# Kernel optimization log

Hardware: AMD Instinct MI355X
Metric: run time of the kernel (lower is better)

The kernel has to match this reference:

```python
import jax, jax.numpy as jnp
import numpy as np

B, H, W, C = 16, 64, 64, 256
NH = 8          # num_heads
WS = 8          # window size (8,8) from shift=2
HID = 1024      # mlp hidden = 4*C
EPS = 1e-5


def _rel_index():
    # relative_position_index exactly as in the torch module (meshgrid 'ij')
    ch = np.arange(WS)
    coords = np.stack(np.meshgrid(ch, ch, indexing='ij'))          # (2, WS, WS)
    flat = coords.reshape(2, -1)                                    # (2, N)
    rel = flat[:, :, None] - flat[:, None, :]                       # (2, N, N)
    rel = rel.transpose(1, 2, 0).astype(np.int64)                   # (N, N, 2)
    rel[..., 0] += WS - 1
    rel[..., 1] += WS - 1
    rel[..., 0] *= 2 * WS - 1
    return jnp.asarray(rel.sum(-1))                                 # (N, N)


def _ln(x, w, b):
    m = x.mean(-1, keepdims=True)
    v = jnp.mean((x - m) ** 2, axis=-1, keepdims=True)
    return (x - m) / jnp.sqrt(v + EPS) * w + b


def setup_inputs() -> dict:
    key = jax.random.key(0)
    ks = jax.random.split(key, 16)
    std = 0.02
    n_bias = (2 * WS - 1) * (2 * WS - 1)  # 225
    return {
        'x': jax.random.normal(ks[0], (B, H * W, C), jnp.float32),
        'norm1_w': jnp.ones((C,), jnp.float32),
        'norm1_b': jnp.zeros((C,), jnp.float32),
        'qkv_w': jax.random.normal(ks[1], (3 * C, C), jnp.float32) * std,
        'qkv_b': jnp.zeros((3 * C,), jnp.float32),
        'rel_bias': jax.random.normal(ks[2], (n_bias, NH), jnp.float32) * std,
        'proj_w': jax.random.normal(ks[3], (C, C), jnp.float32) * std,
        'proj_b': jnp.zeros((C,), jnp.float32),
        'norm2_w': jnp.ones((C,), jnp.float32),
        'norm2_b': jnp.zeros((C,), jnp.float32),
        'fc1_w': jax.random.normal(ks[4], (HID, C), jnp.float32) * std,
        'fc1_b': jnp.zeros((HID,), jnp.float32),
        'dw_w': jax.random.normal(ks[5], (3, 3, 1, HID), jnp.float32) * std,  # HWIO depthwise
        'dw_b': jnp.zeros((HID,), jnp.float32),
        'fc2_w': jax.random.normal(ks[6], (C, HID), jnp.float32) * std,
        'fc2_b': jnp.zeros((C,), jnp.float32),
    }


def reference(x, norm1_w, norm1_b, qkv_w, qkv_b, rel_bias, proj_w, proj_b,
              norm2_w, norm2_b, fc1_w, fc1_b, dw_w, dw_b, fc2_w, fc2_b):
    S = (H // WS) * (W // WS)   # num windows = 64
    N = WS * WS                 # tokens per window = 64
    shortcut = x
    h = _ln(x, norm1_w, norm1_b).reshape(B, H, W, C)
    # window partition -> (B, S, N, C), then permute to (B, N, S, C)
    hw = (h.reshape(B, H // WS, WS, W // WS, WS, C)
            .transpose(0, 1, 3, 2, 4, 5)
            .reshape(B, S, N, C))
    xw = hw.transpose(0, 2, 1, 3)            # (B, N, S, C)
    # qkv over flattened (N*S) tokens; heads split the S*C feature dim
    xf = xw.reshape(B, N * S, C)
    qkv = xf @ qkv_w.T + qkv_b               # (B, N*S, 3C)
    qkv = qkv.reshape(B, N, 3, NH, S * C // NH).transpose(2, 0, 3, 1, 4)
    q, k, v = qkv[0], qkv[1], qkv[2]         # (B, NH, N, S*C/NH)
    scale = (C // NH) ** -0.5
    attn = jnp.einsum('bhnd,bhmd->bhnm', q, k) * scale   # (B, NH, N, N)
    idx = _rel_index()
    bias = rel_bias[idx.reshape(-1)].reshape(N, N, NH).transpose(2, 0, 1)
    attn = jax.nn.softmax(attn + bias[None], axis=-1)
    out = jnp.einsum('bhnm,bhmd->bhnd', attn, v)         # (B, NH, N, S*C/NH)
    out = out.transpose(0, 2, 1, 3).reshape(B, N * S, C)
    out = (out @ proj_w.T + proj_b).reshape(B, N, S, C).transpose(0, 2, 1, 3)  # (B,S,N,C)
    # window reverse -> (B, H*W, C)
    xr = (out.reshape(B, H // WS, W // WS, WS, WS, C)
             .transpose(0, 1, 3, 2, 4, 5)
             .reshape(B, H * W, C))
    x = shortcut + xr
    # conv-based MLP (eval mode, dropout = identity)
    y = _ln(x, norm2_w, norm2_b).reshape(B, H, H, C)      # NHWC
    y = jnp.einsum('bhwc,oc->bhwo', y, fc1_w) + fc1_b     # 1x1 conv
    y = jax.lax.conv_general_dilated(
        y, dw_w, (1, 1), 'SAME',
        dimension_numbers=('NHWC', 'HWIO', 'NHWC'),
        feature_group_count=HID) + dw_b
    y = jax.nn.gelu(y, approximate=False)
    y = jnp.einsum('bhwo,co->bhwc', y, fc2_w) + fc2_b     # 1x1 conv
    return x + y.reshape(B, H * W, C)
```

## Files before the change

### kernel.cpp

```cpp
#include <hip/hip_runtime.h>
#include <hip/hip_bf16.h>
#include <cstdint>
#include <cstddef>

#define B_     16
#define HW_    4096
#define C_     256
#define NH_    8
#define S_     64
#define N_     64
#define C3_    768
#define HID_   1024
#define DHEAD_ 2048
#define EPS_   1e-5f

using u16 = unsigned short;
using u32 = unsigned int;

typedef __attribute__((ext_vector_type(8))) short bf16x8;
typedef __attribute__((ext_vector_type(4))) float f32x4;

__device__ __forceinline__ float bf2f(u16 u) {
  union { float f; u32 i; } x; x.i = ((u32)u) << 16; return x.f;
}
__device__ __forceinline__ u16 f2bf(float f) {
  union { float f; u32 i; } x; x.f = f;
  u32 r = (x.i + 0x7FFFu + ((x.i >> 16) & 1u)) >> 16;
  return (u16)r;
}

__device__ __forceinline__ void gload_lds16(const u16* g, u16* l) {
  __builtin_amdgcn_global_load_lds(
      (const __attribute__((address_space(1))) unsigned int*)g,
      (__attribute__((address_space(3))) unsigned int*)l, 16, 0, 0);
}

__launch_bounds__(256)
__global__ void f2bf_kernel(const float* __restrict__ in, u16* __restrict__ out) {
  int i = blockIdx.x * 256 + threadIdx.x;
  float4 v = ((const float4*)in)[i];
  ushort4 o = {f2bf(v.x), f2bf(v.y), f2bf(v.z), f2bf(v.w)};
  ((ushort4*)out)[i] = o;
}

__launch_bounds__(256)
__global__ void ln_kernel(const float* __restrict__ in, const float* __restrict__ w,
                          const float* __restrict__ bias, u16* __restrict__ out,
                          int b_base) {
  int wave = threadIdx.x >> 6;
  int lane = threadIdx.x & 63;
  int t = blockIdx.x * 4 + wave;
  int b = b_base + (t >> 12);
  int r = t & 4095;
  int n = r >> 6, s = r & 63;
  int hw = (((s >> 3) << 3) + (n >> 3)) * 64 + ((s & 7) << 3) + (n & 7);
  size_t src_row = ((size_t)b << 12) + hw;
  float4 v = ((const float4*)(in + src_row * C_))[lane];
  float sum = v.x + v.y + v.z + v.w;
#pragma unroll
  for (int off = 32; off; off >>= 1) sum += __shfl_xor(sum, off);
  float mean = sum * (1.0f / C_);
  float4 d = {v.x - mean, v.y - mean, v.z - mean, v.w - mean};
  float ss = d.x * d.x + d.y * d.y + d.z * d.z + d.w * d.w;
#pragma unroll
  for (int off = 32; off; off >>= 1) ss += __shfl_xor(ss, off);
  float rstd = rsqrtf(ss * (1.0f / C_) + EPS_);
  float4 w4 = ((const float4*)w)[lane];
  float4 b4 = ((const float4*)bias)[lane];
  ushort4 o;
  o.x = f2bf(d.x * rstd * w4.x + b4.x);
  o.y = f2bf(d.y * rstd * w4.y + b4.y);
  o.z = f2bf(d.z * rstd * w4.z + b4.z);
  o.w = f2bf(d.w * rstd * w4.w + b4.w);
  ((ushort4*)(out + (size_t)t * C_))[lane] = o;
}

template<int K_, int J_, int EPI>
__launch_bounds__(256, 2)
__global__ void gemm_mfma(const u16* __restrict__ A, const u16* __restrict__ Wb,
                          const float* __restrict__ bias, u16* __restrict__ outB,
                          float* __restrict__ outF, const float* __restrict__ res,
                          int m_base, u16* __restrict__ qb, u16* __restrict__ kb,
                          u16* __restrict__ vt) {
  constexpr int NT = K_ / 64;
  __shared__ u16 As[2][128 * 64];
  __shared__ u16 Bs[2][128 * 64];
  int tid = threadIdx.x;
  int wid = tid >> 6, lane = tid & 63;
  int n0 = blockIdx.x * 128;
  int m0 = blockIdx.y * 128;
  int wr = wid >> 1, wc = wid & 1;
  f32x4 acc[4][4] = {};

  int srow8 = lane >> 3;
  int sslot = lane & 7;

#define GSTAGE(buf, t)                                                         \
  {                                                                            \
    int k0g = (t) * 64;                                                        \
    _Pragma("unroll")                                                          \
    for (int r = 0; r < 4; ++r) {                                              \
      int row = wid * 32 + r * 8 + srow8;                                      \
      int cb = ((sslot ^ srow8) << 4);                                         \
      gload_lds16(A + (size_t)(m0 + row) * K_ + k0g + (cb >> 1),               \
                  &As[buf][(wid * 32 + r * 8) * 64]);                          \
      gload_lds16(Wb + (size_t)(n0 + row) * K_ + k0g + (cb >> 1),              \
                  &Bs[buf][(wid * 32 + r * 8) * 64]);                          \
    }                                                                          \
  }

  GSTAGE(0, 0);
  asm volatile("s_waitcnt vmcnt(0)" ::: "memory");
  __builtin_amdgcn_sched_barrier(0);
  __builtin_amdgcn_s_barrier();
  __builtin_amdgcn_sched_barrier(0);

#pragma unroll
  for (int t = 0; t < NT; ++t) {
    if (t + 1 < NT) GSTAGE((t + 1) & 1, t + 1);
    const u16* as = As[t & 1];
    const u16* bs = Bs[t & 1];
#pragma unroll
    for (int kk = 0; kk < 2; ++kk) {
      bf16x8 afr[4], bfr[4];
#pragma unroll
      for (int mf = 0; mf < 4; ++mf) {
        int ra = wr * 64 + mf * 16 + (lane & 15);
        int cb = (((kk * 4 + (lane >> 4)) ^ (ra & 7)) << 4);
        afr[mf] = *(const bf16x8*)&as[ra * 64 + (cb >> 1)];
      }
#pragma unroll
      for (int nf = 0; nf < 4; ++nf) {
        int rb = wc * 64 + nf * 16 + (lane & 15);
        int cb = (((kk * 4 + (lane >> 4)) ^ (rb & 7)) << 4);
        bfr[nf] = *(const bf16x8*)&bs[rb * 64 + (cb >> 1)];
      }
#pragma unroll
      for (int mf = 0; mf < 4; ++mf)
#pragma unroll
        for (int nf = 0; nf < 4; ++nf)
          acc[mf][nf] = __builtin_amdgcn_mfma_f32_16x16x32_bf16(afr[mf], bfr[nf], acc[mf][nf], 0, 0, 0);
    }
    asm volatile("s_waitcnt vmcnt(0)" ::: "memory");
    __builtin_amdgcn_sched_barrier(0);
    __builtin_amdgcn_s_barrier();
    __builtin_amdgcn_sched_barrier(0);
  }
#undef GSTAGE

#pragma unroll
  for (int nf = 0; nf < 4; ++nf) {
    int col = n0 + wc * 64 + nf * 16 + (lane & 15);
    float bv = bias[col];
#pragma unroll
    for (int mf = 0; mf < 4; ++mf) {
#pragma unroll
      for (int j = 0; j < 4; ++j) {
        int m = m0 + wr * 64 + mf * 16 + (lane >> 4) * 4 + j;
        float v = acc[mf][nf][j] + bv;
        if (EPI == 0) {
          outB[(size_t)m * J_ + col] = f2bf(v);
        } else if (EPI == 2) {
          size_t o = (size_t)(m_base + m) * C_ + col;
          outF[o] += v;
        } else {
          int b_rel = m >> 12, nn = (m >> 6) & 63, s = m & 63;
          int f = s * 768 + col;
          int part = f >> 14, hh = (f >> 11) & 7, d = f & 2047;
          u16 val = f2bf(v);
          size_t bh = (size_t)b_rel * 8 + hh;
          if (part == 0)      qb[(bh * 64 + nn) * 2048 + d] = val;
          else if (part == 1) kb[(bh * 64 + nn) * 2048 + d] = val;
          else                vt[(bh * 2048 + d) * 64 + nn] = val;
        }
      }
    }
  }
}

__launch_bounds__(256, 2)
__global__ void proj_ln_fused(const u16* __restrict__ A, const u16* __restrict__ Wb,
                              const float* __restrict__ bias, const float* __restrict__ res,
                              float* __restrict__ outF, const float* __restrict__ ln_w,
                              const float* __restrict__ ln_b, u16* __restrict__ h2,
                              int m_base) {
  __shared__ u16 As[2][64 * 64];
  __shared__ u16 Bs[2][256 * 64];
  int tid = threadIdx.x;
  int wid = tid >> 6, lane = tid & 63;
  int m0 = blockIdx.x * 64;
  f32x4 acc[4][4] = {};
  int srow8 = lane >> 3, sslot = lane & 7;

#define PSTAGE(buf, t)                                                         \
  {                                                                            \
    int k0g = (t) * 64;                                                        \
    int cb = ((sslot ^ srow8) << 4);                                           \
    _Pragma("unroll")                                                          \
    for (int r = 0; r < 2; ++r) {                                              \
      int row = wid * 16 + r * 8 + srow8;                                      \
      gload_lds16(A + (size_t)(m0 + row) * 256 + k0g + (cb >> 1),              \
                  &As[buf][(wid * 16 + r * 8) * 64]);                          \
    }                                                                          \
    _Pragma("unroll")                                                          \
    for (int r = 0; r < 8; ++r) {                                              \
      int row = wid * 64 + r * 8 + srow8;                                      \
      gload_lds16(Wb + (size_t)row * 256 + k0g + (cb >> 1),                    \
                  &Bs[buf][(wid * 64 + r * 8) * 64]);                          \
    }                                                                          \
  }

  PSTAGE(0, 0);
  asm volatile("s_waitcnt vmcnt(0)" ::: "memory");
  __builtin_amdgcn_sched_barrier(0);
  __builtin_amdgcn_s_barrier();
  __builtin_amdgcn_sched_barrier(0);

#pragma unroll
  for (int t = 0; t < 4; ++t) {
    if (t + 1 < 4) PSTAGE((t + 1) & 1, t + 1);
    const u16* as = As[t & 1];
    const u16* bs = Bs[t & 1];
#pragma unroll
    for (int kk = 0; kk < 2; ++kk) {
      bf16x8 afr[4], bfr[4];
#pragma unroll
      for (int mf = 0; mf < 4; ++mf) {
        int ra = mf * 16 + (lane & 15);
        int cb = (((kk * 4 + (lane >> 4)) ^ (ra & 7)) << 4);
        afr[mf] = *(const bf16x8*)&as[ra * 64 + (cb >> 1)];
      }
#pragma unroll
      for (int nf = 0; nf < 4; ++nf) {
        int rb = wid * 64 + nf * 16 + (lane & 15);
        int cb = (((kk * 4 + (lane >> 4)) ^ (rb & 7)) << 4);
        bfr[nf] = *(const bf16x8*)&bs[rb * 64 + (cb >> 1)];
      }
#pragma unroll
      for (int mf = 0; mf < 4; ++mf)
#pragma unroll
        for (int nf = 0; nf < 4; ++nf)
          acc[mf][nf] = __builtin_amdgcn_mfma_f32_16x16x32_bf16(afr[mf], bfr[nf], acc[mf][nf], 0, 0, 0);
    }
    asm volatile("s_waitcnt vmcnt(0)" ::: "memory");
    __builtin_amdgcn_sched_barrier(0);
    __builtin_amdgcn_s_barrier();
    __builtin_amdgcn_sched_barrier(0);
  }
#undef PSTAGE

  float (*red)[8] = (float (*)[8])As;

#pragma unroll
  for (int mf = 0; mf < 4; ++mf) {
#pragma unroll
    for (int j = 0; j < 4; ++j) {
      int m = m0 + mf * 16 + (lane >> 4) * 4 + j;
      int gm = m_base + m;
      int b = gm >> 12, nn = (gm >> 6) & 63, s = gm & 63;
      int hw = (((s >> 3) << 3) + (nn >> 3)) * 64 + ((s & 7) << 3) + (nn & 7);
      size_t rowo = (((size_t)b << 12) + hw) * C_;
      float s1 = 0.f, s2 = 0.f;
#pragma unroll
      for (int nf = 0; nf < 4; ++nf) {
        int col = wid * 64 + nf * 16 + (lane & 15);
        float v = acc[mf][nf][j] + bias[col] + res[rowo + col];
        acc[mf][nf][j] = v;
        outF[rowo + col] = v;
        s1 += v; s2 += v * v;
      }
#pragma unroll
      for (int off = 1; off < 16; off <<= 1) {
        s1 += __shfl_xor(s1, off);
        s2 += __shfl_xor(s2, off);
      }
      if ((lane & 15) == 0) {
        int rr = mf * 16 + (lane >> 4) * 4 + j;
        red[rr][wid * 2] = s1;
        red[rr][wid * 2 + 1] = s2;
      }
    }
  }
  __syncthreads();

#pragma unroll
  for (int mf = 0; mf < 4; ++mf) {
#pragma unroll
    for (int j = 0; j < 4; ++j) {
      int rr = mf * 16 + (lane >> 4) * 4 + j;
      float sum = red[rr][0] + red[rr][2] + red[rr][4] + red[rr][6];
      float ssq = red[rr][1] + red[rr][3] + red[rr][5] + red[rr][7];
      float mean = sum * (1.0f / C_);
      float var = ssq * (1.0f / C_) - mean * mean;
      float rstd = rsqrtf(var + EPS_);
      int m = m0 + rr;
      int b_rel = m >> 12, nn = (m >> 6) & 63, s = m & 63;
      int hw = (((s >> 3) << 3) + (nn >> 3)) * 64 + ((s & 7) << 3) + (nn & 7);
      size_t ho = (((size_t)b_rel << 12) + hw) * C_;
#pragma unroll
      for (int nf = 0; nf < 4; ++nf) {
        int col = wid * 64 + nf * 16 + (lane & 15);
        float nv = (acc[mf][nf][j] - mean) * rstd * ln_w[col] + ln_b[col];
        h2[ho + col] = f2bf(nv);
      }
    }
  }
}

__launch_bounds__(256)
__global__ void attn_mfma(const u16* __restrict__ qb, const u16* __restrict__ kb,
                          const u16* __restrict__ vt, const float* __restrict__ rel_bias,
                          u16* __restrict__ outp) {
  __shared__ u16 bufA[4096];
  __shared__ u16 bufB[4096];
  int bh = blockIdx.x;
  int h = bh & 7;
  int b_rel = bh >> 3;
  int tid = threadIdx.x;
  int w = tid >> 6, lane = tid & 63;
  int l3 = lane >> 3, l7 = lane & 7;
  const u16* qg = qb + (size_t)bh * 64 * 2048;
  const u16* kg = kb + (size_t)bh * 64 * 2048;
  const u16* vg = vt + (size_t)bh * 2048 * 64;

  f32x4 acc[4] = {};
  for (int k0 = 0; k0 < 2048; k0 += 64) {
#pragma unroll
    for (int r = 0; r < 2; ++r) {
      int row = w * 16 + r * 8 + l3;
      int sc = (l7 ^ (row & 7)) * 8;
      gload_lds16(qg + (size_t)row * 2048 + k0 + sc, &bufA[(w * 16 + r * 8) * 64]);
      gload_lds16(kg + (size_t)row * 2048 + k0 + sc, &bufB[(w * 16 + r * 8) * 64]);
    }
    __syncthreads();
    int rowq = w * 16 + (lane & 15);
#pragma unroll
    for (int ks = 0; ks < 2; ++ks) {
      bf16x8 aq = *(const bf16x8*)&bufA[rowq * 64 + (((ks * 4 + (lane >> 4)) ^ (rowq & 7)) << 3)];
#pragma unroll
      for (int cf = 0; cf < 4; ++cf) {
        int m = cf * 16 + (lane & 15);
        bf16x8 bk = *(const bf16x8*)&bufB[m * 64 + (((ks * 4 + (lane >> 4)) ^ (m & 7)) << 3)];
        acc[cf] = __builtin_amdgcn_mfma_f32_16x16x32_bf16(aq, bk, acc[cf], 0, 0, 0);
      }
    }
    __syncthreads();
  }

  const float scale = 0.17677669529663688f;
#pragma unroll
  for (int j = 0; j < 4; ++j) {
    int r = w * 16 + (lane >> 4) * 4 + j;
    int i1 = r >> 3, j1 = r & 7;
    float v[4];
#pragma unroll
    for (int cf = 0; cf < 4; ++cf) {
      int c = cf * 16 + (lane & 15);
      int idx = (i1 - (c >> 3) + 7) * 15 + (j1 - (c & 7) + 7);
      v[cf] = acc[cf][j] * scale + rel_bias[idx * NH_ + h];
    }
    float mx = fmaxf(fmaxf(v[0], v[1]), fmaxf(v[2], v[3]));
#pragma unroll
    for (int off = 8; off; off >>= 1) mx = fmaxf(mx, __shfl_xor(mx, off));
    float sm = 0.f;
#pragma unroll
    for (int cf = 0; cf < 4; ++cf) { v[cf] = __expf(v[cf] - mx); sm += v[cf]; }
#pragma unroll
    for (int off = 8; off; off >>= 1) sm += __shfl_xor(sm, off);
    float inv = 1.0f / sm;
#pragma unroll
    for (int cf = 0; cf < 4; ++cf) {
      int c = cf * 16 + (lane & 15);
      bufA[r * 64 + (c ^ ((r & 7) << 3))] = f2bf(v[cf] * inv);
    }
  }
  __syncthreads();

  bf16x8 pa[2];
  {
    int n = w * 16 + (lane & 15);
#pragma unroll
    for (int ks = 0; ks < 2; ++ks)
      pa[ks] = *(const bf16x8*)&bufA[n * 64 + ((ks * 32 + (lane >> 4) * 8) ^ ((n & 7) << 3))];
  }

  for (int d0 = 0; d0 < 2048; d0 += 64) {
#pragma unroll
    for (int r = 0; r < 2; ++r) {
      int drow = w * 16 + r * 8 + l3;
      int sc = (l7 ^ (drow & 7)) * 8;
      gload_lds16(vg + (size_t)(d0 + drow) * 64 + sc, &bufB[(w * 16 + r * 8) * 64]);
    }
    __syncthreads();
    f32x4 o[4] = {};
#pragma unroll
    for (int ks = 0; ks < 2; ++ks)
#pragma unroll
      for (int cf = 0; cf < 4; ++cf) {
        int d = cf * 16 + (lane & 15);
        bf16x8 bv = *(const bf16x8*)&bufB[d * 64 + (((ks * 4 + (lane >> 4)) ^ (d & 7)) << 3)];
        o[cf] = __builtin_amdgcn_mfma_f32_16x16x32_bf16(pa[ks], bv, o[cf], 0, 0, 0);
      }
#pragma unroll
    for (int cf = 0; cf < 4; ++cf) {
      int f = h * 2048 + d0 + cf * 16 + (lane & 15);
      int s = f >> 8, c = f & 255;
#pragma unroll
      for (int j = 0; j < 4; ++j) {
        int n = w * 16 + (lane >> 4) * 4 + j;
        outp[(((size_t)b_rel * 64 + n) * 64 + s) * 256 + c] = f2bf(o[cf][j]);
      }
    }
    __syncthreads();
  }
}

__launch_bounds__(256)
__global__ void dwconv_gelu(const u16* __restrict__ y1, const float* __restrict__ dw_w,
                            const float* __restrict__ dw_b, u16* __restrict__ y2) {
  int bid = blockIdx.x;
  int wt = bid & 31, ht = (bid >> 5) & 15, b = bid >> 9;
  int h0 = ht * 4, w0 = wt * 2;
  int c0 = threadIdx.x * 4;

  float4 wv[9];
#pragma unroll
  for (int i = 0; i < 9; ++i) wv[i] = *(const float4*)&dw_w[i * HID_ + c0];

  ushort4 in[6][4];
#pragma unroll
  for (int ii = 0; ii < 6; ++ii) {
    int hh = h0 + ii - 1;
#pragma unroll
    for (int jj = 0; jj < 4; ++jj) {
      int ww = w0 + jj - 1;
      if ((unsigned)hh < 64u && (unsigned)ww < 64u)
        in[ii][jj] = *(const ushort4*)(y1 + ((size_t)((b << 12) + hh * 64 + ww)) * HID_ + c0);
      else
        in[ii][jj] = ushort4{0, 0, 0, 0};
    }
  }

  float4 bv = *(const float4*)&dw_b[c0];
  float4 acc[4][2];
#pragma unroll
  for (int i = 0; i < 4; ++i)
#pragma unroll
    for (int j = 0; j < 2; ++j) acc[i][j] = bv;

#pragma unroll
  for (int ii = 0; ii < 6; ++ii) {
#pragma unroll
    for (int jj = 0; jj < 4; ++jj) {
      ushort4 u = in[ii][jj];
      float4 f = {bf2f(u.x), bf2f(u.y), bf2f(u.z), bf2f(u.w)};
#pragma unroll
      for (int kh = 0; kh < 3; ++kh) {
        int i = ii - kh;
        if (i < 0 || i > 3) continue;
#pragma unroll
        for (int kw = 0; kw < 3; ++kw) {
          int j = jj - kw;
          if (j < 0 || j > 1) continue;
          float4 w4 = wv[kh * 3 + kw];
          acc[i][j].x += f.x * w4.x;
          acc[i][j].y += f.y * w4.y;
          acc[i][j].z += f.z * w4.z;
          acc[i][j].w += f.w * w4.w;
        }
      }
    }
  }

  const float k = 0.70710678118654752f;
#pragma unroll
  for (int i = 0; i < 4; ++i) {
#pragma unroll
    for (int j = 0; j < 2; ++j) {
      float4 a = acc[i][j];
      ushort4 o;
      o.x = f2bf(0.5f * a.x * (1.0f + erff(a.x * k)));
      o.y = f2bf(0.5f * a.y * (1.0f + erff(a.y * k)));
      o.z = f2bf(0.5f * a.z * (1.0f + erff(a.z * k)));
      o.w = f2bf(0.5f * a.w * (1.0f + erff(a.w * k)));
      *(ushort4*)(y2 + ((size_t)((b << 12) + (h0 + i) * 64 + (w0 + j))) * HID_ + c0) = o;
    }
  }
}

extern "C" void kernel_launch(void* const* d_in, const int* in_sizes, int n_in,
                              void* d_out, int out_size, void* d_ws, size_t ws_size,
                              hipStream_t stream) {
  const float* x       = (const float*)d_in[0];
  const float* norm1_w = (const float*)d_in[1];
  const float* norm1_b = (const float*)d_in[2];
  const float* qkv_w   = (const float*)d_in[3];
  const float* qkv_b   = (const float*)d_in[4];
  const float* rel_b   = (const float*)d_in[5];
  const float* proj_w  = (const float*)d_in[6];
  const float* proj_b  = (const float*)d_in[7];
  const float* norm2_w = (const float*)d_in[8];
  const float* norm2_b = (const float*)d_in[9];
  const float* fc1_w   = (const float*)d_in[10];
  const float* fc1_b   = (const float*)d_in[11];
  const float* dw_w    = (const float*)d_in[12];
  const float* dw_b    = (const float*)d_in[13];
  const float* fc2_w   = (const float*)d_in[14];
  const float* fc2_b   = (const float*)d_in[15];
  float* out = (float*)d_out;
  char* ws = (char*)d_ws;

  u16* wq = (u16*)(ws);
  u16* wp = wq + 768 * 256;
  u16* w1 = wp + 256 * 256;
  u16* w2 = w1 + 1024 * 256;
  f2bf_kernel<<<768 * 256 / 1024, 256, 0, stream>>>(qkv_w, wq);
  f2bf_kernel<<<256 * 256 / 1024, 256, 0, stream>>>(proj_w, wp);
  f2bf_kernel<<<1024 * 256 / 1024, 256, 0, stream>>>(fc1_w, w1);
  f2bf_kernel<<<1024 * 256 / 1024, 256, 0, stream>>>(fc2_w, w2);

  const size_t MBy = (size_t)1 << 20;
  char* cws = ws + 2 * MBy;
  int G = 1;
  for (int g = 16; g >= 1; g >>= 1) {
    if (2 * MBy + (size_t)(18 * g) * MBy <= ws_size) { G = g; break; }
  }
  const size_t gm = (size_t)G * MBy;
  u16* h1c    = (u16*)(cws);
  u16* qbuf   = (u16*)(cws + 2 * gm);
  u16* kbuf   = (u16*)(cws + 4 * gm);
  u16* vtbuf  = (u16*)(cws + 6 * gm);
  u16* attnoc = (u16*)(cws + 8 * gm);
  u16* h2c    = (u16*)(cws);
  u16* y1c    = (u16*)(cws + 2 * gm);
  u16* y2c    = (u16*)(cws + 10 * gm);

  const int Mloc = G * 4096;
  for (int b0 = 0; b0 < B_; b0 += G) {
    ln_kernel<<<Mloc / 4, 256, 0, stream>>>(x, norm1_w, norm1_b, h1c, b0);
    gemm_mfma<256, 768, 3><<<dim3(6, Mloc / 128), 256, 0, stream>>>(
        h1c, wq, qkv_b, nullptr, nullptr, nullptr, 0, qbuf, kbuf, vtbuf);
    attn_mfma<<<G * 8, 256, 0, stream>>>(qbuf, kbuf, vtbuf, rel_b, attnoc);
    proj_ln_fused<<<Mloc / 64, 256, 0, stream>>>(
        attnoc, wp, proj_b, x, out, norm2_w, norm2_b, h2c, b0 * 4096);
    gemm_mfma<256, 1024, 0><<<dim3(8, Mloc / 128), 256, 0, stream>>>(
        h2c, w1, fc1_b, y1c, nullptr, nullptr, 0, nullptr, nullptr, nullptr);
    dwconv_gelu<<<Mloc / 8, 256, 0, stream>>>(y1c, dw_w, dw_b, y2c);
    gemm_mfma<1024, 256, 2><<<dim3(2, Mloc / 128), 256, 0, stream>>>(
        y2c, w2, fc2_b, nullptr, out, nullptr, b0 * 4096, nullptr, nullptr, nullptr);
  }
}
```

Baseline: 541.6 us.

## Pre-pack weights into MFMA fragment layout and load B directly from global

Weights are converted to bf16 in a fragment-major packed layout, so each lane can read its 16-byte MFMA B fragment straight from global memory (L2-resident). This removes the B tile LDS staging and the LDS reads in the QKV/fc GEMM and the proj+LN kernel, which cuts LDS traffic and footprint, and the occupancy hint of 2 is dropped from launch bounds. In exchange every block re-reads the weights from global/L2 per k-step, and those register loads are exposed latency ahead of the MFMAs. Register pressure also rises because eight B fragments are held per k-tile.

```diff
diff --git a/kernel.cpp b/kernel.cpp
--- a/kernel.cpp
+++ b/kernel.cpp
@@ -36,11 +36,23 @@
 }
 
 __launch_bounds__(256)
-__global__ void f2bf_kernel(const float* __restrict__ in, u16* __restrict__ out) {
-  int i = blockIdx.x * 256 + threadIdx.x;
-  float4 v = ((const float4*)in)[i];
-  ushort4 o = {f2bf(v.x), f2bf(v.y), f2bf(v.z), f2bf(v.w)};
-  ((ushort4*)out)[i] = o;
+__global__ void pack_w_kernel(const float* __restrict__ W, u16* __restrict__ out,
+                              int K, int kshift) {
+  int g = blockIdx.x * 256 + threadIdx.x;
+  int lane = g & 63;
+  int pk = g >> 6;
+  int cb = pk >> kshift;
+  int kb = pk & ((1 << kshift) - 1);
+  int j = cb * 16 + (lane & 15);
+  int k = kb * 32 + ((lane >> 4) << 3);
+  const float* src = W + (size_t)j * K + k;
+  float4 a = ((const float4*)src)[0];
+  float4 b = ((const float4*)src)[1];
+  ushort4 lo = {f2bf(a.x), f2bf(a.y), f2bf(a.z), f2bf(a.w)};
+  ushort4 hi = {f2bf(b.x), f2bf(b.y), f2bf(b.z), f2bf(b.w)};
+  ushort4* dst = (ushort4*)(out + (size_t)g * 8);
+  dst[0] = lo;
+  dst[1] = hi;
 }
 
 __launch_bounds__(256)
@@ -76,77 +88,71 @@
 }
 
 template<int K_, int J_, int EPI>
-__launch_bounds__(256, 2)
-__global__ void gemm_mfma(const u16* __restrict__ A, const u16* __restrict__ Wb,
+__launch_bounds__(256)
+__global__ void gemm_mfma(const u16* __restrict__ A, const u16* __restrict__ wpk,
                           const float* __restrict__ bias, u16* __restrict__ outB,
                           float* __restrict__ outF, const float* __restrict__ res,
                           int m_base, u16* __restrict__ qb, u16* __restrict__ kb,
                           u16* __restrict__ vt) {
   constexpr int NT = K_ / 64;
   __shared__ u16 As[2][128 * 64];
-  __shared__ u16 Bs[2][128 * 64];
   int tid = threadIdx.x;
   int wid = tid >> 6, lane = tid & 63;
   int n0 = blockIdx.x * 128;
   int m0 = blockIdx.y * 128;
   int wr = wid >> 1, wc = wid & 1;
   f32x4 acc[4][4] = {};
-
-  int srow8 = lane >> 3;
-  int sslot = lane & 7;
-
-#define GSTAGE(buf, t)                                                         \
+  int srow8 = lane >> 3, sslot = lane & 7;
+
+#define ASTAGE(buf, t)                                                         \
   {                                                                            \
     int k0g = (t) * 64;                                                        \
+    int cbb = ((sslot ^ srow8) << 4);                                          \
     _Pragma("unroll")                                                          \
     for (int r = 0; r < 4; ++r) {                                              \
       int row = wid * 32 + r * 8 + srow8;                                      \
-      int cb = ((sslot ^ srow8) << 4);                                         \
-      gload_lds16(A + (size_t)(m0 + row) * K_ + k0g + (cb >> 1),               \
+      gload_lds16(A + (size_t)(m0 + row) * K_ + k0g + (cbb >> 1),              \
                   &As[buf][(wid * 32 + r * 8) * 64]);                          \
-      gload_lds16(Wb + (size_t)(n0 + row) * K_ + k0g + (cb >> 1),              \
-                  &Bs[buf][(wid * 32 + r * 8) * 64]);                          \
     }                                                                          \
   }
 
-  GSTAGE(0, 0);
+  ASTAGE(0, 0);
   asm volatile("s_waitcnt vmcnt(0)" ::: "memory");
   __builtin_amdgcn_sched_barrier(0);
   __builtin_amdgcn_s_barrier();
   __builtin_amdgcn_sched_barrier(0);
 
-#pragma unroll
   for (int t = 0; t < NT; ++t) {
-    if (t + 1 < NT) GSTAGE((t + 1) & 1, t + 1);
+    bf16x8 bfr[8];
+#pragma unroll
+    for (int kk = 0; kk < 2; ++kk)
+#pragma unroll
+      for (int nf = 0; nf < 4; ++nf)
+        bfr[kk * 4 + nf] = *(const bf16x8*)&wpk[
+            ((size_t)(((n0 >> 4) + wc * 4 + nf) * (K_ / 32) + (t * 2 + kk)) * 64 + lane) * 8];
+    if (t + 1 < NT) ASTAGE((t + 1) & 1, t + 1);
     const u16* as = As[t & 1];
-    const u16* bs = Bs[t & 1];
 #pragma unroll
     for (int kk = 0; kk < 2; ++kk) {
-      bf16x8 afr[4], bfr[4];
+      bf16x8 afr[4];
 #pragma unroll
       for (int mf = 0; mf < 4; ++mf) {
         int ra = wr * 64 + mf * 16 + (lane & 15);
-        int cb = (((kk * 4 + (lane >> 4)) ^ (ra & 7)) << 4);
-        afr[mf] = *(const bf16x8*)&as[ra * 64 + (cb >> 1)];
-      }
-#pragma unroll
-      for (int nf = 0; nf < 4; ++nf) {
-        int rb = wc * 64 + nf * 16 + (lane & 15);
-        int cb = (((kk * 4 + (lane >> 4)) ^ (rb & 7)) << 4);
-        bfr[nf] = *(const bf16x8*)&bs[rb * 64 + (cb >> 1)];
+        int cbb = (((kk * 4 + (lane >> 4)) ^ (ra & 7)) << 4);
+        afr[mf] = *(const bf16x8*)&as[ra * 64 + (cbb >> 1)];
       }
 #pragma unroll
       for (int mf = 0; mf < 4; ++mf)
 #pragma unroll
         for (int nf = 0; nf < 4; ++nf)
-          acc[mf][nf] = __builtin_amdgcn_mfma_f32_16x16x32_bf16(afr[mf], bfr[nf], acc[mf][nf], 0, 0, 0);
+          acc[mf][nf] = __builtin_amdgcn_mfma_f32_16x16x32_bf16(afr[mf], bfr[kk * 4 + nf], acc[mf][nf], 0, 0, 0);
     }
     asm volatile("s_waitcnt vmcnt(0)" ::: "memory");
     __builtin_amdgcn_sched_barrier(0);
     __builtin_amdgcn_s_barrier();
     __builtin_amdgcn_sched_barrier(0);
   }
-#undef GSTAGE
+#undef ASTAGE
 
 #pragma unroll
   for (int nf = 0; nf < 4; ++nf) {
@@ -178,14 +184,14 @@
   }
 }
 
-__launch_bounds__(256, 2)
-__global__ void proj_ln_fused(const u16* __restrict__ A, const u16* __restrict__ Wb,
+__launch_bounds__(256)
+__global__ void proj_ln_fused(const u16* __restrict__ A, const u16* __restrict__ wpk,
                               const float* __restrict__ bias, const float* __restrict__ res,
                               float* __restrict__ outF, const float* __restrict__ ln_w,
                               const float* __restrict__ ln_b, u16* __restrict__ h2,
                               int m_base) {
   __shared__ u16 As[2][64 * 64];
-  __shared__ u16 Bs[2][256 * 64];
+  __shared__ float red[64][8];
   int tid = threadIdx.x;
   int wid = tid >> 6, lane = tid & 63;
   int m0 = blockIdx.x * 64;
@@ -195,18 +201,12 @@
 #define PSTAGE(buf, t)                                                         \
   {                                                                            \
     int k0g = (t) * 64;                                                        \
-    int cb = ((sslot ^ srow8) << 4);                                           \
+    int cbb = ((sslot ^ srow8) << 4);                                          \
     _Pragma("unroll")                                                          \
     for (int r = 0; r < 2; ++r) {                                              \
       int row = wid * 16 + r * 8 + srow8;                                      \
-      gload_lds16(A + (size_t)(m0 + row) * 256 + k0g + (cb >> 1),              \
+      gload_lds16(A + (size_t)(m0 + row) * 256 + k0g + (cbb >> 1),             \
                   &As[buf][(wid * 16 + r * 8) * 64]);                          \
-    }                                                                          \
-    _Pragma("unroll")                                                          \
-    for (int r = 0; r < 8; ++r) {                                              \
-      int row = wid * 64 + r * 8 + srow8;                                      \
-      gload_lds16(Wb + (size_t)row * 256 + k0g + (cb >> 1),                    \
-                  &Bs[buf][(wid * 64 + r * 8) * 64]);                          \
     }                                                                          \
   }
 
@@ -218,29 +218,29 @@
 
 #pragma unroll
   for (int t = 0; t < 4; ++t) {
+    bf16x8 bfr[8];
+#pragma unroll
+    for (int kk = 0; kk < 2; ++kk)
+#pragma unroll
+      for (int nf = 0; nf < 4; ++nf)
+        bfr[kk * 4 + nf] = *(const bf16x8*)&wpk[
+            ((size_t)((wid * 4 + nf) * 8 + (t * 2 + kk)) * 64 + lane) * 8];
     if (t + 1 < 4) PSTAGE((t + 1) & 1, t + 1);
     const u16* as = As[t & 1];
-    const u16* bs = Bs[t & 1];
 #pragma unroll
     for (int kk = 0; kk < 2; ++kk) {
-      bf16x8 afr[4], bfr[4];
+      bf16x8 afr[4];
 #pragma unroll
       for (int mf = 0; mf < 4; ++mf) {
         int ra = mf * 16 + (lane & 15);
-        int cb = (((kk * 4 + (lane >> 4)) ^ (ra & 7)) << 4);
-        afr[mf] = *(const bf16x8*)&as[ra * 64 + (cb >> 1)];
-      }
-#pragma unroll
-      for (int nf = 0; nf < 4; ++nf) {
-        int rb = wid * 64 + nf * 16 + (lane & 15);
-        int cb = (((kk * 4 + (lane >> 4)) ^ (rb & 7)) << 4);
-        bfr[nf] = *(const bf16x8*)&bs[rb * 64 + (cb >> 1)];
+        int cbb = (((kk * 4 + (lane >> 4)) ^ (ra & 7)) << 4);
+        afr[mf] = *(const bf16x8*)&as[ra * 64 + (cbb >> 1)];
       }
 #pragma unroll
       for (int mf = 0; mf < 4; ++mf)
 #pragma unroll
         for (int nf = 0; nf < 4; ++nf)
-          acc[mf][nf] = __builtin_amdgcn_mfma_f32_16x16x32_bf16(afr[mf], bfr[nf], acc[mf][nf], 0, 0, 0);
+          acc[mf][nf] = __builtin_amdgcn_mfma_f32_16x16x32_bf16(afr[mf], bfr[kk * 4 + nf], acc[mf][nf], 0, 0, 0);
     }
     asm volatile("s_waitcnt vmcnt(0)" ::: "memory");
     __builtin_amdgcn_sched_barrier(0);
@@ -248,8 +248,6 @@
     __builtin_amdgcn_sched_barrier(0);
   }
 #undef PSTAGE
-
-  float (*red)[8] = (float (*)[8])As;
 
 #pragma unroll
   for (int mf = 0; mf < 4; ++mf) {
@@ -514,10 +512,10 @@
   u16* wp = wq + 768 * 256;
   u16* w1 = wp + 256 * 256;
   u16* w2 = w1 + 1024 * 256;
-  f2bf_kernel<<<768 * 256 / 1024, 256, 0, stream>>>(qkv_w, wq);
-  f2bf_kernel<<<256 * 256 / 1024, 256, 0, stream>>>(proj_w, wp);
-  f2bf_kernel<<<1024 * 256 / 1024, 256, 0, stream>>>(fc1_w, w1);
-  f2bf_kernel<<<1024 * 256 / 1024, 256, 0, stream>>>(fc2_w, w2);
+  pack_w_kernel<<<768 * 256 / 8 / 256, 256, 0, stream>>>(qkv_w, wq, 256, 3);
+  pack_w_kernel<<<256 * 256 / 8 / 256, 256, 0, stream>>>(proj_w, wp, 256, 3);
+  pack_w_kernel<<<1024 * 256 / 8 / 256, 256, 0, stream>>>(fc1_w, w1, 256, 3);
+  pack_w_kernel<<<256 * 1024 / 8 / 256, 256, 0, stream>>>(fc2_w, w2, 1024, 5);
 
   const size_t MBy = (size_t)1 << 20;
   char* cws = ws + 2 * MBy;
```

Result: no change. 533.0 us (-1.6%).
